# Kernel tuning notes

Measured on AMD Instinct MI355X. Metric: run time of the kernel, lower is better.

## Reference

```python
import jax, jax.numpy as jnp
import numpy as np
from jax import lax

EPS = 1e-5
DN = ('NCDHW', 'OIDHW', 'NCDHW')


def _instance_norm(x, w, b):
    # normalize over spatial dims per (batch, channel); biased variance like torch
    mu = jnp.mean(x, axis=(2, 3, 4), keepdims=True)
    var = jnp.mean((x - mu) ** 2, axis=(2, 3, 4), keepdims=True)
    xn = (x - mu) * lax.rsqrt(var + EPS)
    return xn * w[None, :, None, None, None] + b[None, :, None, None, None]


def _conv1x1(x, w, b):
    # w: [Cout, Cin]
    y = jnp.einsum('bcdhw,oc->bodhw', x, w)
    return y + b[None, :, None, None, None]


def _dwconv3(x, w, b):
    # depthwise 3x3x3, padding 1; w: [C, 1, 3, 3, 3]
    y = lax.conv_general_dilated(x, w, (1, 1, 1), 'SAME',
                                 dimension_numbers=DN,
                                 feature_group_count=w.shape[0])
    return y + b[None, :, None, None, None]


def setup_inputs() -> dict:
    key = jax.random.key(0)
    ks = jax.random.split(key, 8)
    C, half = 64, 32
    B, D, H, W = 1, 96, 96, 96
    s1 = 1.0 / np.sqrt(C)          # fan_in of 1x1 conv
    s3 = 1.0 / np.sqrt(27.0)       # fan_in of depthwise 3x3x3
    return {
        'x': jax.random.normal(ks[0], (B, C, D, H, W), jnp.float32),
        'norm_w': jnp.ones((C,), jnp.float32),
        'norm_b': jnp.zeros((C,), jnp.float32),
        'in_proj_w': jax.random.normal(ks[1], (C, C), jnp.float32) * s1,
        'in_proj_b': jnp.zeros((C,), jnp.float32),
        'conv_ssm_w': jax.random.normal(ks[2], (half, 1, 3, 3, 3), jnp.float32) * s3,
        'conv_ssm_b': jnp.zeros((half,), jnp.float32),
        'mamba_w': jax.random.normal(ks[3], (half, 1, 3, 3, 3), jnp.float32) * s3,
        'mamba_b': jnp.zeros((half,), jnp.float32),
        'conv_sym_w': jax.random.normal(ks[4], (half, 1, 3, 3, 3), jnp.float32) * s3,
        'conv_sym_b': jnp.zeros((half,), jnp.float32),
        'out_proj_w': jax.random.normal(ks[5], (C, C), jnp.float32) * s1,
        'out_proj_b': jnp.zeros((C,), jnp.float32),
    }


def reference(x, norm_w, norm_b, in_proj_w, in_proj_b,
              conv_ssm_w, conv_ssm_b, mamba_w, mamba_b,
              conv_sym_w, conv_sym_b, out_proj_w, out_proj_b):
    residual = x
    xp = _conv1x1(_instance_norm(x, norm_w, norm_b), in_proj_w, in_proj_b)
    half = xp.shape[1] // 2
    x1, x2 = xp[:, :half], xp[:, half:]
    # SSM branch (TriDirectionalMamba fallback = depthwise conv3)
    x1 = _dwconv3(jax.nn.silu(_dwconv3(x1, conv_ssm_w, conv_ssm_b)), mamba_w, mamba_b)
    # symmetric conv branch
    x2 = jax.nn.silu(_dwconv3(x2, conv_sym_w, conv_sym_b))
    y = _conv1x1(jnp.concatenate([x1, x2], axis=1), out_proj_w, out_proj_b)
    return y + residual
```

## Files before the change

kernel.cpp:

```cpp
#include <hip/hip_runtime.h>

typedef unsigned short u16;
typedef unsigned int u32;
typedef short bf16x8 __attribute__((ext_vector_type(8)));
typedef float f32x16 __attribute__((ext_vector_type(16)));
typedef u16 u16x8 __attribute__((ext_vector_type(8)));

#define DIM 96
#define PLANE (DIM*DIM)
#define S 884736
#define C 64
#define HALF 32
#define PARTS 16
#define EPS 1e-5f
#define DSPLIT 4
#define DCHUNK (DIM/DSPLIT)

#define MFMA32(a,b,c) __builtin_amdgcn_mfma_f32_32x32x16_bf16(a,b,c,0,0,0)

__device__ __forceinline__ u16 f2bf(float f) {
  u32 u = __builtin_bit_cast(u32, f);
  return (u16)((u + 0x7FFFu + ((u >> 16) & 1u)) >> 16);
}
__device__ __forceinline__ float bf2f(u16 h) {
  return __builtin_bit_cast(float, (u32)h << 16);
}
__device__ __forceinline__ u32 cvt_pk_bf16(float lo, float hi) {
  u32 r;
  asm("v_cvt_pk_bf16_f32 %0, %1, %2" : "=v"(r) : "v"(lo), "v"(hi));
  return r;
}
__device__ __forceinline__ float silu(float v) { return v / (1.f + __expf(-v)); }
__device__ __forceinline__ u16x8 zero8() {
  u16x8 z;
  #pragma unroll
  for (int i = 0; i < 8; ++i) z[i] = 0;
  return z;
}

__global__ __launch_bounds__(256) void k1_stats(const float* __restrict__ x,
                                                u16* __restrict__ xb,
                                                float* __restrict__ psum,
                                                float* __restrict__ psq) {
  const int bid = blockIdx.x;
  const int ch = bid / PARTS, part = bid % PARTS;
  const int chunk = S / PARTS;
  const size_t base = (size_t)ch * S + (size_t)part * chunk;
  const float4* p = (const float4*)(x + base);
  ushort4* xb4 = (ushort4*)(xb + base);
  const int n4 = chunk / 4;
  float s = 0.f, q = 0.f;
  for (int i = threadIdx.x; i < n4; i += 256) {
    float4 v = p[i];
    s += (v.x + v.y) + (v.z + v.w);
    q += (v.x * v.x + v.y * v.y) + (v.z * v.z + v.w * v.w);
    union { u32 u[2]; ushort4 v4; } o;
    o.u[0] = cvt_pk_bf16(v.x, v.y);
    o.u[1] = cvt_pk_bf16(v.z, v.w);
    xb4[i] = o.v4;
  }
  #pragma unroll
  for (int off = 32; off > 0; off >>= 1) {
    s += __shfl_down(s, off);
    q += __shfl_down(q, off);
  }
  __shared__ float ls[4], lq[4];
  const int wid = threadIdx.x >> 6, lane = threadIdx.x & 63;
  if (lane == 0) { ls[wid] = s; lq[wid] = q; }
  __syncthreads();
  if (threadIdx.x == 0) {
    psum[bid] = (ls[0] + ls[1]) + (ls[2] + ls[3]);
    psq[bid]  = (lq[0] + lq[1]) + (lq[2] + lq[3]);
  }
}

__global__ __launch_bounds__(64) void k1b_prep(const float* __restrict__ psum,
    const float* __restrict__ psq,
    const float* __restrict__ norm_w, const float* __restrict__ norm_b,
    const float* __restrict__ in_w, const float* __restrict__ in_b,
    const float* __restrict__ out_w,
    u16* __restrict__ Wp, float* __restrict__ biasp, u16* __restrict__ Wo) {
  __shared__ float a_s[C], b2_s[C];
  const int t = threadIdx.x;
  float s = 0.f, q = 0.f;
  for (int i = 0; i < PARTS; ++i) { s += psum[t * PARTS + i]; q += psq[t * PARTS + i]; }
  const float inv = 1.f / (float)S;
  const float mu = s * inv;
  const float var = q * inv - mu * mu;
  const float rsig = rsqrtf(var + EPS);
  const float a = norm_w[t] * rsig;
  const float b2 = norm_b[t] - mu * a;
  a_s[t] = a; b2_s[t] = b2;
  __syncthreads();
  float bp = in_b[t];
  for (int c = 0; c < C; ++c) {
    const float w = in_w[t * C + c];
    Wp[t * C + c] = f2bf(w * a_s[c]);
    bp += b2_s[c] * w;
    Wo[t * C + c] = f2bf(out_w[t * C + c]);
  }
  biasp[t] = bp;
}

__global__ __launch_bounds__(256) void k2_mfma(const u16* __restrict__ xb,
    const u16* __restrict__ Wp, const float* __restrict__ biasp,
    u16* __restrict__ xp) {
  const int lane = threadIdx.x & 63, wid = threadIdx.x >> 6;
  const int n = lane & 31, hf = lane >> 5;
  const int v0 = blockIdx.x * 256 + wid * 64;
  bf16x8 A[2][4];
  #pragma unroll
  for (int t = 0; t < 2; ++t)
    #pragma unroll
    for (int s = 0; s < 4; ++s)
      A[t][s] = *(const bf16x8*)(Wp + (t * 32 + n) * C + s * 16 + hf * 8);

  f32x16 accE[2], accO[2];
  #pragma unroll
  for (int t = 0; t < 2; ++t)
    #pragma unroll
    for (int r = 0; r < 16; ++r) {
      const float b = biasp[t * 32 + (r & 3) + 8 * (r >> 2) + 4 * hf];
      accE[t][r] = b; accO[t][r] = b;
    }

  #pragma unroll
  for (int s = 0; s < 4; ++s) {
    union { u16 u[8]; bf16x8 v; } BE, BO;
    #pragma unroll
    for (int j = 0; j < 8; ++j) {
      const u32 xv = *(const u32*)(xb + (size_t)(s * 16 + hf * 8 + j) * S + v0 + 2 * n);
      BE.u[j] = (u16)(xv & 0xFFFFu); BO.u[j] = (u16)(xv >> 16);
    }
    #pragma unroll
    for (int t = 0; t < 2; ++t) {
      accE[t] = MFMA32(A[t][s], BE.v, accE[t]);
      accO[t] = MFMA32(A[t][s], BO.v, accO[t]);
    }
  }
  #pragma unroll
  for (int t = 0; t < 2; ++t)
    #pragma unroll
    for (int r = 0; r < 16; ++r) {
      const int o = t * 32 + (r & 3) + 8 * (r >> 2) + 4 * hf;
      *(u32*)(xp + (size_t)o * S + v0 + 2 * n) = cvt_pk_bf16(accE[t][r], accO[t][r]);
    }
}

__device__ __forceinline__ void fma_row8(float* __restrict__ a,
    const float* __restrict__ r, float t0, float t1, float t2) {
  #pragma unroll
  for (int i = 0; i < 8; ++i) a[i] += t0 * r[i] + t1 * r[i + 1] + t2 * r[i + 2];
}

template<bool SILU>
__global__ __launch_bounds__(192, 2) void dwconv(const u16* __restrict__ srcA,
    const float* __restrict__ kwA, const float* __restrict__ bA,
    u16* __restrict__ dstA,
    const float* __restrict__ kwB, const float* __restrict__ bB,
    u16* __restrict__ dstB) {
  const int c = blockIdx.z;
  const u16* src = srcA + (size_t)c * S;
  u16* dst; const float* kwp; float bias;
  if (c < HALF) { dst = dstA + (size_t)c * S;          kwp = kwA + c * 27;          bias = bA[c]; }
  else          { dst = dstB + (size_t)(c - HALF) * S; kwp = kwB + (c - HALF) * 27; bias = bB[c - HALF]; }
  float kw[27];
  #pragma unroll
  for (int i = 0; i < 27; ++i) kw[i] = kwp[i];

  const int w8 = threadIdx.x * 8;
  const int h  = blockIdx.x * 16 + threadIdx.y;
  const bool hm = h > 0, hp = h < DIM - 1;
  const bool wlo = w8 > 0, whi = w8 < DIM - 8;
  const int d0 = blockIdx.y * DCHUNK;

  u16x8 Rm[3]; u16 Rlo[3], Rhi[3];
  float r0[10], r1[10], r2[10];
  float A[8], B[8], o8[8];

  #define RAWLOAD(PPTR) { \
    const u16* _p = (PPTR); \
    if (hm) { Rm[0] = *(const u16x8*)(_p - DIM); Rlo[0] = wlo ? _p[-DIM - 1] : (u16)0; Rhi[0] = whi ? _p[-DIM + 8] : (u16)0; } \
    else    { Rm[0] = zero8(); Rlo[0] = 0; Rhi[0] = 0; } \
    {         Rm[1] = *(const u16x8*)(_p);       Rlo[1] = wlo ? _p[-1]       : (u16)0; Rhi[1] = whi ? _p[8]        : (u16)0; } \
    if (hp) { Rm[2] = *(const u16x8*)(_p + DIM); Rlo[2] = wlo ? _p[DIM - 1]  : (u16)0; Rhi[2] = whi ? _p[DIM + 8]  : (u16)0; } \
    else    { Rm[2] = zero8(); Rlo[2] = 0; Rhi[2] = 0; } }

  #define CONVERT() { \
    r0[0] = bf2f(Rlo[0]); r1[0] = bf2f(Rlo[1]); r2[0] = bf2f(Rlo[2]); \
    _Pragma("unroll") \
    for (int i = 0; i < 8; ++i) { \
      r0[1 + i] = bf2f(Rm[0][i]); r1[1 + i] = bf2f(Rm[1][i]); r2[1 + i] = bf2f(Rm[2][i]); } \
    r0[9] = bf2f(Rhi[0]); r1[9] = bf2f(Rhi[1]); r2[9] = bf2f(Rhi[2]); }

  #define CBLK(ACC, K0) \
    fma_row8(ACC, r0, kw[(K0) + 0], kw[(K0) + 1], kw[(K0) + 2]); \
    fma_row8(ACC, r1, kw[(K0) + 3], kw[(K0) + 4], kw[(K0) + 5]); \
    fma_row8(ACC, r2, kw[(K0) + 6], kw[(K0) + 7], kw[(K0) + 8]);

  const u16* pb0 = src + h * DIM + w8;

  if (d0 > 0) {
    RAWLOAD(pb0 + (size_t)(d0 - 1) * PLANE); CONVERT();
    #pragma unroll
    for (int i = 0; i < 8; ++i) B[i] = bias;
    CBLK(B, 0);
  } else {
    #pragma unroll
    for (int i = 0; i < 8; ++i) B[i] = bias;
  }
  RAWLOAD(pb0 + (size_t)d0 * PLANE); CONVERT();
  #pragma unroll
  for (int i = 0; i < 8; ++i) { A[i] = B[i]; B[i] = bias; }
  CBLK(A, 9);
  CBLK(B, 0);
  const u16* pb = pb0 + (size_t)(d0 + 1) * PLANE;
  RAWLOAD(pb);
  u16* db = dst + (size_t)d0 * PLANE + h * DIM + w8;

  #pragma unroll 1
  for (int d = d0; d < d0 + DCHUNK; ++d) {
    if (d + 1 < DIM) { CONVERT(); }
    else {
      #pragma unroll
      for (int i = 0; i < 10; ++i) { r0[i] = 0.f; r1[i] = 0.f; r2[i] = 0.f; }
    }
    pb += PLANE;
    if (d + 2 < DIM) RAWLOAD(pb);
    #pragma unroll
    for (int i = 0; i < 8; ++i) o8[i] = A[i];
    CBLK(o8, 18);
    #pragma unroll
    for (int i = 0; i < 8; ++i) A[i] = B[i];
    CBLK(A, 9);
    #pragma unroll
    for (int i = 0; i < 8; ++i) B[i] = bias;
    CBLK(B, 0);
    if (SILU) {
      #pragma unroll
      for (int i = 0; i < 8; ++i) o8[i] = silu(o8[i]);
    }
    union { u32 u[4]; u16x8 v; } o;
    #pragma unroll
    for (int i = 0; i < 4; ++i) o.u[i] = cvt_pk_bf16(o8[2 * i], o8[2 * i + 1]);
    *(u16x8*)db = o.v;
    db += PLANE;
  }
  #undef CBLK
  #undef CONVERT
  #undef RAWLOAD
}

__global__ __launch_bounds__(256) void k4b_mfma(const u16* __restrict__ z_lo,
    const u16* __restrict__ z_hi, const u16* __restrict__ xb,
    const u16* __restrict__ Wo, const float* __restrict__ ob,
    float* __restrict__ out) {
  const int lane = threadIdx.x & 63, wid = threadIdx.x >> 6;
  const int n = lane & 31, hf = lane >> 5;
  const int v0 = blockIdx.x * 256 + wid * 64;
  bf16x8 A[2][4];
  #pragma unroll
  for (int t = 0; t < 2; ++t)
    #pragma unroll
    for (int s = 0; s < 4; ++s)
      A[t][s] = *(const bf16x8*)(Wo + (t * 32 + n) * C + s * 16 + hf * 8);

  f32x16 accE[2], accO[2];
  #pragma unroll
  for (int t = 0; t < 2; ++t)
    #pragma unroll
    for (int r = 0; r < 16; ++r) {
      const float b = ob[t * 32 + (r & 3) + 8 * (r >> 2) + 4 * hf];
      accE[t][r] = b; accO[t][r] = b;
    }

  #pragma unroll
  for (int s = 0; s < 4; ++s) {
    const u16* zbase = (s < 2) ? z_lo + (size_t)(s * 16) * S
                               : z_hi + (size_t)((s - 2) * 16) * S;
    union { u16 u[8]; bf16x8 v; } BE, BO;
    #pragma unroll
    for (int j = 0; j < 8; ++j) {
      const u32 zv = *(const u32*)(zbase + (size_t)(hf * 8 + j) * S + v0 + 2 * n);
      BE.u[j] = (u16)(zv & 0xFFFFu); BO.u[j] = (u16)(zv >> 16);
    }
    #pragma unroll
    for (int t = 0; t < 2; ++t) {
      accE[t] = MFMA32(A[t][s], BE.v, accE[t]);
      accO[t] = MFMA32(A[t][s], BO.v, accO[t]);
    }
  }
  #pragma unroll
  for (int t = 0; t < 2; ++t)
    #pragma unroll
    for (int r = 0; r < 16; ++r) {
      const int o = t * 32 + (r & 3) + 8 * (r >> 2) + 4 * hf;
      const u32 xr = *(const u32*)(xb + (size_t)o * S + v0 + 2 * n);
      float2 ov;
      ov.x = accE[t][r] + bf2f((u16)(xr & 0xFFFFu));
      ov.y = accO[t][r] + bf2f((u16)(xr >> 16));
      *(float2*)(out + (size_t)o * S + v0 + 2 * n) = ov;
    }
}

extern "C" void kernel_launch(void* const* d_in, const int* in_sizes, int n_in,
                              void* d_out, int out_size, void* d_ws, size_t ws_size,
                              hipStream_t stream) {
  const float* x      = (const float*)d_in[0];
  const float* norm_w = (const float*)d_in[1];
  const float* norm_b = (const float*)d_in[2];
  const float* in_w   = (const float*)d_in[3];
  const float* in_b   = (const float*)d_in[4];
  const float* ssm_w  = (const float*)d_in[5];
  const float* ssm_b  = (const float*)d_in[6];
  const float* mam_w  = (const float*)d_in[7];
  const float* mam_b  = (const float*)d_in[8];
  const float* sym_w  = (const float*)d_in[9];
  const float* sym_b  = (const float*)d_in[10];
  const float* out_w  = (const float*)d_in[11];
  const float* out_b  = (const float*)d_in[12];
  float* out = (float*)d_out;

  u16* xb   = (u16*)d_ws;
  u16* xp   = xb + (size_t)C * S;
  u16* t1   = xp + (size_t)C * S;
  u16* z_hi = t1 + (size_t)HALF * S;
  u16* z_lo = xp;
  float* psum  = (float*)(z_hi + (size_t)HALF * S);
  float* psq   = psum + C * PARTS;
  u16* Wp      = (u16*)(psq + C * PARTS);
  u16* Wo      = Wp + C * C;
  float* biasp = (float*)(Wo + C * C);

  k1_stats<<<C * PARTS, 256, 0, stream>>>(x, xb, psum, psq);
  k1b_prep<<<1, 64, 0, stream>>>(psum, psq, norm_w, norm_b, in_w, in_b, out_w,
                                 Wp, biasp, Wo);
  k2_mfma<<<S / 256, 256, 0, stream>>>(xb, Wp, biasp, xp);
  dwconv<true><<<dim3(DIM / 16, DSPLIT, C), dim3(12, 16, 1), 0, stream>>>(
      xp, ssm_w, ssm_b, t1, sym_w, sym_b, z_hi);
  dwconv<false><<<dim3(DIM / 16, DSPLIT, HALF), dim3(12, 16, 1), 0, stream>>>(
      t1, mam_w, mam_b, z_lo, mam_w, mam_b, z_lo);
  k4b_mfma<<<S / 256, 256, 0, stream>>>(z_lo, z_hi, xb, Wo, out_b, out);
}
```

Before: 402.3 us.

## Double-buffer depthwise conv plane loads with two-plane prefetch distance

The depthwise 3x3x3 conv kernel now keeps two register buffers of raw bf16 plane rows and unrolls the depth loop by two. Each buffer is loaded two planes ahead, so global loads have more time in flight behind the FMA work. The launch-bounds hint that requested two blocks per SIMD is removed, which lets the compiler use more registers for the extra buffer. The cost is higher register pressure and possibly lower occupancy, which could hurt latency hiding in this memory-heavy kernel.

```diff
diff --git a/kernel.cpp b/kernel.cpp
--- a/kernel.cpp
+++ b/kernel.cpp
@@ -154,7 +154,7 @@
 }
 
 template<bool SILU>
-__global__ __launch_bounds__(192, 2) void dwconv(const u16* __restrict__ srcA,
+__global__ __launch_bounds__(192) void dwconv(const u16* __restrict__ srcA,
     const float* __restrict__ kwA, const float* __restrict__ bA,
     u16* __restrict__ dstA,
     const float* __restrict__ kwB, const float* __restrict__ bB,
@@ -174,34 +174,59 @@
   const bool wlo = w8 > 0, whi = w8 < DIM - 8;
   const int d0 = blockIdx.y * DCHUNK;
 
-  u16x8 Rm[3]; u16 Rlo[3], Rhi[3];
+  u16x8 Qm[3]; u16 Qlo[3], Qhi[3];
+  u16x8 Pm[3]; u16 Plo[3], Phi[3];
   float r0[10], r1[10], r2[10];
   float A[8], B[8], o8[8];
 
-  #define RAWLOAD(PPTR) { \
+  #define RAWLOAD(M, LO, HI, PPTR) { \
     const u16* _p = (PPTR); \
-    if (hm) { Rm[0] = *(const u16x8*)(_p - DIM); Rlo[0] = wlo ? _p[-DIM - 1] : (u16)0; Rhi[0] = whi ? _p[-DIM + 8] : (u16)0; } \
-    else    { Rm[0] = zero8(); Rlo[0] = 0; Rhi[0] = 0; } \
-    {         Rm[1] = *(const u16x8*)(_p);       Rlo[1] = wlo ? _p[-1]       : (u16)0; Rhi[1] = whi ? _p[8]        : (u16)0; } \
-    if (hp) { Rm[2] = *(const u16x8*)(_p + DIM); Rlo[2] = wlo ? _p[DIM - 1]  : (u16)0; Rhi[2] = whi ? _p[DIM + 8]  : (u16)0; } \
-    else    { Rm[2] = zero8(); Rlo[2] = 0; Rhi[2] = 0; } }
-
-  #define CONVERT() { \
-    r0[0] = bf2f(Rlo[0]); r1[0] = bf2f(Rlo[1]); r2[0] = bf2f(Rlo[2]); \
+    if (hm) { M[0] = *(const u16x8*)(_p - DIM); LO[0] = wlo ? _p[-DIM - 1] : (u16)0; HI[0] = whi ? _p[-DIM + 8] : (u16)0; } \
+    else    { M[0] = zero8(); LO[0] = 0; HI[0] = 0; } \
+    {         M[1] = *(const u16x8*)(_p);       LO[1] = wlo ? _p[-1]       : (u16)0; HI[1] = whi ? _p[8]        : (u16)0; } \
+    if (hp) { M[2] = *(const u16x8*)(_p + DIM); LO[2] = wlo ? _p[DIM - 1]  : (u16)0; HI[2] = whi ? _p[DIM + 8]  : (u16)0; } \
+    else    { M[2] = zero8(); LO[2] = 0; HI[2] = 0; } }
+
+  #define CONVERT(M, LO, HI) { \
+    r0[0] = bf2f(LO[0]); r1[0] = bf2f(LO[1]); r2[0] = bf2f(LO[2]); \
     _Pragma("unroll") \
     for (int i = 0; i < 8; ++i) { \
-      r0[1 + i] = bf2f(Rm[0][i]); r1[1 + i] = bf2f(Rm[1][i]); r2[1 + i] = bf2f(Rm[2][i]); } \
-    r0[9] = bf2f(Rhi[0]); r1[9] = bf2f(Rhi[1]); r2[9] = bf2f(Rhi[2]); }
+      r0[1 + i] = bf2f(M[0][i]); r1[1 + i] = bf2f(M[1][i]); r2[1 + i] = bf2f(M[2][i]); } \
+    r0[9] = bf2f(HI[0]); r1[9] = bf2f(HI[1]); r2[9] = bf2f(HI[2]); }
+
+  #define ZROWS() { \
+    _Pragma("unroll") \
+    for (int i = 0; i < 10; ++i) { r0[i] = 0.f; r1[i] = 0.f; r2[i] = 0.f; } }
 
   #define CBLK(ACC, K0) \
     fma_row8(ACC, r0, kw[(K0) + 0], kw[(K0) + 1], kw[(K0) + 2]); \
     fma_row8(ACC, r1, kw[(K0) + 3], kw[(K0) + 4], kw[(K0) + 5]); \
     fma_row8(ACC, r2, kw[(K0) + 6], kw[(K0) + 7], kw[(K0) + 8]);
 
+  #define COMPUTE_STORE() { \
+    _Pragma("unroll") \
+    for (int i = 0; i < 8; ++i) o8[i] = A[i]; \
+    CBLK(o8, 18); \
+    _Pragma("unroll") \
+    for (int i = 0; i < 8; ++i) A[i] = B[i]; \
+    CBLK(A, 9); \
+    _Pragma("unroll") \
+    for (int i = 0; i < 8; ++i) B[i] = bias; \
+    CBLK(B, 0); \
+    if (SILU) { \
+      _Pragma("unroll") \
+      for (int i = 0; i < 8; ++i) o8[i] = silu(o8[i]); \
+    } \
+    union { u32 u[4]; u16x8 v; } _o; \
+    _Pragma("unroll") \
+    for (int i = 0; i < 4; ++i) _o.u[i] = cvt_pk_bf16(o8[2 * i], o8[2 * i + 1]); \
+    *(u16x8*)db = _o.v; \
+    db += PLANE; }
+
   const u16* pb0 = src + h * DIM + w8;
 
   if (d0 > 0) {
-    RAWLOAD(pb0 + (size_t)(d0 - 1) * PLANE); CONVERT();
+    RAWLOAD(Qm, Qlo, Qhi, pb0 + (size_t)(d0 - 1) * PLANE); CONVERT(Qm, Qlo, Qhi);
     #pragma unroll
     for (int i = 0; i < 8; ++i) B[i] = bias;
     CBLK(B, 0);
@@ -209,44 +234,31 @@
     #pragma unroll
     for (int i = 0; i < 8; ++i) B[i] = bias;
   }
-  RAWLOAD(pb0 + (size_t)d0 * PLANE); CONVERT();
+  RAWLOAD(Qm, Qlo, Qhi, pb0 + (size_t)d0 * PLANE); CONVERT(Qm, Qlo, Qhi);
   #pragma unroll
   for (int i = 0; i < 8; ++i) { A[i] = B[i]; B[i] = bias; }
   CBLK(A, 9);
   CBLK(B, 0);
-  const u16* pb = pb0 + (size_t)(d0 + 1) * PLANE;
-  RAWLOAD(pb);
+  RAWLOAD(Qm, Qlo, Qhi, pb0 + (size_t)(d0 + 1) * PLANE);
+  RAWLOAD(Pm, Plo, Phi, pb0 + (size_t)(d0 + 2) * PLANE);
+  const u16* pA = pb0 + (size_t)(d0 + 3) * PLANE;
+  const u16* pB = pA + PLANE;
   u16* db = dst + (size_t)d0 * PLANE + h * DIM + w8;
 
   #pragma unroll 1
-  for (int d = d0; d < d0 + DCHUNK; ++d) {
-    if (d + 1 < DIM) { CONVERT(); }
-    else {
-      #pragma unroll
-      for (int i = 0; i < 10; ++i) { r0[i] = 0.f; r1[i] = 0.f; r2[i] = 0.f; }
-    }
-    pb += PLANE;
-    if (d + 2 < DIM) RAWLOAD(pb);
-    #pragma unroll
-    for (int i = 0; i < 8; ++i) o8[i] = A[i];
-    CBLK(o8, 18);
-    #pragma unroll
-    for (int i = 0; i < 8; ++i) A[i] = B[i];
-    CBLK(A, 9);
-    #pragma unroll
-    for (int i = 0; i < 8; ++i) B[i] = bias;
-    CBLK(B, 0);
-    if (SILU) {
-      #pragma unroll
-      for (int i = 0; i < 8; ++i) o8[i] = silu(o8[i]);
-    }
-    union { u32 u[4]; u16x8 v; } o;
-    #pragma unroll
-    for (int i = 0; i < 4; ++i) o.u[i] = cvt_pk_bf16(o8[2 * i], o8[2 * i + 1]);
-    *(u16x8*)db = o.v;
-    db += PLANE;
-  }
+  for (int d = d0; d < d0 + DCHUNK; d += 2) {
+    CONVERT(Qm, Qlo, Qhi);
+    if (d + 3 < DIM) { RAWLOAD(Qm, Qlo, Qhi, pA); }
+    pA += 2 * PLANE;
+    COMPUTE_STORE();
+    if (d + 2 < DIM) { CONVERT(Pm, Plo, Phi); } else { ZROWS(); }
+    if (d + 4 < DIM) { RAWLOAD(Pm, Plo, Phi, pB); }
+    pB += 2 * PLANE;
+    COMPUTE_STORE();
+  }
+  #undef COMPUTE_STORE
   #undef CBLK
+  #undef ZROWS
   #undef CONVERT
   #undef RAWLOAD
 }
```

Measured after the change: 387.4 us. -3.7%, faster.
